# Kernel tuning notes

Measured on AMD Instinct MI355X. Metric: run time of the kernel, lower is better.

## Reference

```python
import jax, jax.numpy as jnp
import numpy as np

N_NODES = 100000
N_EDGES = 1000000
IN_FEATS = 64
HID = 128
NUM_CLASSES = 10


def setup_inputs() -> dict:
    key = jax.random.key(0)
    ks = jax.random.split(key, 8)
    x = jax.random.normal(ks[0], (N_NODES, IN_FEATS), dtype=jnp.float32)
    edge_index = jax.random.randint(ks[1], (2, N_EDGES), 0, N_NODES, dtype=jnp.int64)
    # Glorot-style init scale for weights
    def w(k, fan_in, fan_out):
        s = (2.0 / (fan_in + fan_out)) ** 0.5
        return jax.random.normal(k, (fan_in, fan_out), dtype=jnp.float32) * s
    return {
        "x": x,
        "edge_index": edge_index,
        "W1": w(ks[2], IN_FEATS, HID),
        "b1": jnp.zeros((HID,), dtype=jnp.float32),
        "W2": w(ks[3], HID, HID),
        "b2": jnp.zeros((HID,), dtype=jnp.float32),
        "Wl": w(ks[4], HID, NUM_CLASSES),
        "bl": jnp.zeros((NUM_CLASSES,), dtype=jnp.float32),
    }


def _gcn_conv(x, src, dst, norm, W, b, num_nodes):
    # PyG GCNConv: h = x W, then out_i = sum_{j->i} norm_ij * h_j + b
    h = x @ W  # [N, out]
    msgs = h[src] * norm[:, None]  # gather + scale  [E+N, out]
    out = jax.ops.segment_sum(msgs, dst, num_segments=num_nodes)
    return out + b


def reference(x, edge_index, W1, b1, W2, b2, Wl, bl):
    N = x.shape[0]
    loops = jnp.arange(N, dtype=edge_index.dtype)
    src = jnp.concatenate([edge_index[0], loops])  # source nodes (messages from)
    dst = jnp.concatenate([edge_index[1], loops])  # target nodes (aggregate at)
    # symmetric normalization: deg over targets (includes self-loops)
    deg = jax.ops.segment_sum(jnp.ones(dst.shape, dtype=x.dtype), dst, num_segments=N)
    dinv = jnp.where(deg > 0, jax.lax.rsqrt(deg), 0.0)
    norm = dinv[src] * dinv[dst]  # [E+N]

    h = jax.nn.relu(_gcn_conv(x, src, dst, norm, W1, b1, N))
    h = jax.nn.relu(_gcn_conv(h, src, dst, norm, W2, b2, N))
    return jax.nn.log_softmax(h @ Wl + bl, axis=1)
```

## Files before the change

kernel.cpp:

```cpp
#include <hip/hip_runtime.h>
#include <hip/hip_fp16.h>
#include <math.h>

#define NUM_CLASSES 10

#define BSH 7
#define BSZ 128
#define BCAP 1792
#define NBMAX 1024
#define P1BATCH 4096
#define PREPB 97

typedef _Float16 half8  __attribute__((ext_vector_type(8)));
typedef _Float16 half4t __attribute__((ext_vector_type(4)));
typedef float    floatx4 __attribute__((ext_vector_type(4)));

__global__ __launch_bounds__(256) void prep_p1_kernel(const float* __restrict__ W1,
                                                      const float* __restrict__ W2,
                                                      const float* __restrict__ Wlc,
                                                      _Float16* __restrict__ W1t,
                                                      _Float16* __restrict__ W2t,
                                                      _Float16* __restrict__ Wct,
                                                      const int* __restrict__ src,
                                                      const int* __restrict__ dst,
                                                      int* __restrict__ bucket_fill,
                                                      unsigned* __restrict__ pairs, int E) {
    __shared__ int hist[NBMAX], base[NBMAX], cur[NBMAX];
    const int tid = threadIdx.x;
    const int b = blockIdx.x;

    if (b < PREPB) {
        if (b < 32) {
            int i = b * 256 + tid;
            int k = i >> 7, c = i & 127;
            W1t[c * 72 + k] = (_Float16)W1[i];
        } else if (b < 96) {
            int i = (b - 32) * 256 + tid;
            int k = i >> 7, c = i & 127;
            W2t[c * 136 + k] = (_Float16)W2[i];
        } else {
            for (int i = tid; i < 16 * 136; i += 256) {
                int c = i / 136, k = i - c * 136;
                float v = (c < NUM_CLASSES && k < 128) ? Wlc[k * NUM_CLASSES + c] : 0.0f;
                Wct[i] = (_Float16)v;
            }
        }
        return;
    }

    for (int i = tid; i < NBMAX; i += 256) { hist[i] = 0; cur[i] = 0; }
    __syncthreads();
    const int bb = (b - PREPB) * P1BATCH;
    unsigned pk[16];
    int bk[16];
    int cnt = 0;
#pragma unroll
    for (int i = 0; i < 16; ++i) {
        int idx = bb + i * 256 + tid;
        if (idx < E) {
            int s = src[idx], d = dst[idx];
            bk[i] = d >> BSH;
            pk[i] = ((unsigned)s << BSH) | (unsigned)(d & (BSZ - 1));
            atomicAdd(&hist[bk[i]], 1);
            cnt = i + 1;
        }
    }
    __syncthreads();
    for (int i = tid; i < NBMAX; i += 256)
        if (hist[i] > 0) base[i] = atomicAdd(&bucket_fill[i], hist[i]);
    __syncthreads();
#pragma unroll
    for (int i = 0; i < 16; ++i) {
        if (i < cnt) {
            int bi = bk[i];
            int r = atomicAdd(&cur[bi], 1) + base[bi];
            if (r < BCAP) pairs[(size_t)bi * BCAP + r] = pk[i];
        }
    }
}

__global__ __launch_bounds__(256) void csr_p2_kernel(const int* __restrict__ bucket_fill,
                                                     const unsigned* __restrict__ pairs,
                                                     const float* __restrict__ x,
                                                     int* __restrict__ rowstart,
                                                     float* __restrict__ dinv,
                                                     int* __restrict__ csr_src,
                                                     __half2* __restrict__ xs_h,
                                                     int N, int nbuck) {
    __shared__ int cnt[BSZ], excl[BSZ], cur[BSZ];
    __shared__ int s1[256];
    const int tid = threadIdx.x;
    const int b = blockIdx.x;
    const int node0 = b << BSH;
    const int nodes_b = min(BSZ, N - node0);

    if (tid < BSZ) { cnt[tid] = 0; cur[tid] = 0; }
    int part = 0;
    for (int j = tid; j < b; j += 256) part += bucket_fill[j];
    s1[tid] = part;
    __syncthreads();
    for (int off = 128; off > 0; off >>= 1) {
        if (tid < off) s1[tid] += s1[tid + off];
        __syncthreads();
    }
    const int bbase = s1[0];
    const int ne = bucket_fill[b];
    __syncthreads();

    const unsigned* bp = pairs + (size_t)b * BCAP;
    for (int i = tid; i < ne; i += 256)
        atomicAdd(&cnt[bp[i] & (BSZ - 1)], 1);
    __syncthreads();
    int c = (tid < BSZ) ? cnt[tid] : 0;
    if (tid < BSZ) s1[tid] = c;
    __syncthreads();
    for (int off = 1; off < BSZ; off <<= 1) {
        int t = (tid < BSZ && tid >= off) ? s1[tid - off] : 0;
        __syncthreads();
        if (tid < BSZ) s1[tid] += t;
        __syncthreads();
    }
    if (tid < BSZ) excl[tid] = s1[tid] - c;
    __syncthreads();

    if (tid < nodes_b) {
        rowstart[node0 + tid] = bbase + excl[tid];
        dinv[node0 + tid] = rsqrtf((float)cnt[tid] + 1.0f);
    }
    if (b == nbuck - 1 && tid == 0) rowstart[N] = bbase + ne;

    for (int i = tid; i < nodes_b * 32; i += 256) {
        int ln = i >> 5;
        float d = rsqrtf((float)cnt[ln] + 1.0f);
        float2 v = ((const float2*)x)[(size_t)node0 * 32 + i];
        xs_h[(size_t)node0 * 32 + i] = __floats2half2_rn(v.x * d, v.y * d);
    }
    for (int i = tid; i < ne; i += 256) {
        unsigned p = bp[i];
        int d = (int)(p & (BSZ - 1));
        int r = atomicAdd(&cur[d], 1);
        csr_src[bbase + excl[d] + r] = (int)(p >> BSH);
    }
}

__global__ __launch_bounds__(256) void gather_gemm1_kernel(
        const __half2* __restrict__ xs,
        const float* __restrict__ dinv,
        const int* __restrict__ rowstart,
        const int* __restrict__ csr_src,
        const _Float16* __restrict__ Wt,
        const float* __restrict__ bias,
        _Float16* __restrict__ Out, int N) {
    constexpr int KP = 72;
    __shared__ _Float16 As[16 * KP];
    const int tid = threadIdx.x;
    const int lane = tid & 63;
    const int wave = tid >> 6;
    const int q = lane >> 4;
    const int l15 = lane & 15;

    half8 wfr[2][2];
    floatx4 bvr[2];
#pragma unroll
    for (int tt = 0; tt < 2; ++tt) {
        const int t = wave * 2 + tt;
#pragma unroll
        for (int c = 0; c < 2; ++c)
            wfr[tt][c] = *(const half8*)(Wt + (t * 16 + l15) * KP + c * 32 + q * 8);
        bvr[tt] = *(const floatx4*)(bias + t * 16 + q * 4);
    }

    const int f2 = lane & 31;
    for (int nn = 0; nn < 4; ++nn) {
        const int r = wave * 4 + nn;
        const int node = blockIdx.x * 16 + r;
        if (node < N) {
            int beg = rowstart[node];
            int end = rowstart[node + 1];
            int deg = end - beg;

            float2 self = __half22float2(xs[(size_t)node * 32 + f2]);
            float2 acc;

            if (deg <= 16) {
                int myidx = (lane < deg) ? csr_src[beg + lane] : node;
                float comp = (float)(deg - 15);
                acc.x = self.x * comp;
                acc.y = self.y * comp;
                float2 v[16];
#pragma unroll
                for (int u = 0; u < 16; ++u) {
                    int s = __shfl(myidx, u);
                    v[u] = __half22float2(xs[(size_t)s * 32 + f2]);
                }
#pragma unroll
                for (int u = 0; u < 16; ++u) { acc.x += v[u].x; acc.y += v[u].y; }
            } else {
                int lim = deg < 64 ? deg : 64;
                int myidx = (lane < lim) ? csr_src[beg + lane] : node;
                int itersUp = (lim + 7) & ~7;
                float comp = (float)(1 - (itersUp - lim));
                acc.x = self.x * comp;
                acc.y = self.y * comp;
                for (int j = 0; j < itersUp; j += 8) {
                    int s[8];
#pragma unroll
                    for (int u = 0; u < 8; ++u) s[u] = __shfl(myidx, j + u);
                    float2 v[8];
#pragma unroll
                    for (int u = 0; u < 8; ++u) v[u] = __half22float2(xs[(size_t)s[u] * 32 + f2]);
#pragma unroll
                    for (int u = 0; u < 8; ++u) { acc.x += v[u].x; acc.y += v[u].y; }
                }
                for (int j = beg + 64; j < end; ++j) {
                    float2 v = __half22float2(xs[(size_t)csr_src[j] * 32 + f2]);
                    acc.x += v.x;
                    acc.y += v.y;
                }
            }
            if (lane < 32) {
                float d = dinv[node];
                ((__half2*)As)[r * 36 + f2] = __floats2half2_rn(d * acc.x, d * acc.y);
            }
        }
    }
    __syncthreads();

    half8 xf[2];
#pragma unroll
    for (int c = 0; c < 2; ++c)
        xf[c] = *(const half8*)(As + l15 * KP + c * 32 + q * 8);
    const int myrow = blockIdx.x * 16 + l15;
    float sc = (myrow < N) ? dinv[myrow] : 0.0f;
#pragma unroll
    for (int tt = 0; tt < 2; ++tt) {
        floatx4 acc = (floatx4){0.f, 0.f, 0.f, 0.f};
#pragma unroll
        for (int c = 0; c < 2; ++c)
            acc = __builtin_amdgcn_mfma_f32_16x16x32_f16(wfr[tt][c], xf[c], acc, 0, 0, 0);
        if (myrow < N) {
            const int c0 = (wave * 2 + tt) * 16 + q * 4;
            half4t hh;
#pragma unroll
            for (int j = 0; j < 4; ++j)
                hh[j] = (_Float16)(sc * fmaxf(acc[j] + bvr[tt][j], 0.0f));
            *(half4t*)(Out + (size_t)myrow * 128 + c0) = hh;
        }
    }
}

__global__ __launch_bounds__(256) void gather_gemm_final_kernel(
        const __half2* __restrict__ hs,
        const float* __restrict__ dinv,
        const int* __restrict__ rowstart,
        const int* __restrict__ csr_src,
        const _Float16* __restrict__ Wt,
        const float* __restrict__ bias,
        const _Float16* __restrict__ Wct,
        const float* __restrict__ bl,
        float* __restrict__ out, int N) {
    constexpr int KP = 136;
    __shared__ _Float16 As[16 * KP];
    __shared__ _Float16 H2[16 * KP];
    const int tid = threadIdx.x;
    const int lane = tid & 63;
    const int wave = tid >> 6;
    const int q = lane >> 4;
    const int l15 = lane & 15;

    half8 wfr[2][4];
    floatx4 bvr[2];
#pragma unroll
    for (int tt = 0; tt < 2; ++tt) {
        const int t = wave * 2 + tt;
#pragma unroll
        for (int c = 0; c < 4; ++c)
            wfr[tt][c] = *(const half8*)(Wt + (t * 16 + l15) * KP + c * 32 + q * 8);
        bvr[tt] = *(const floatx4*)(bias + t * 16 + q * 4);
    }

    for (int nn = 0; nn < 4; ++nn) {
        const int r = wave * 4 + nn;
        const int node = blockIdx.x * 16 + r;
        if (node < N) {
            int beg = rowstart[node];
            int end = rowstart[node + 1];
            int deg = end - beg;

            float2 self = __half22float2(hs[(size_t)node * 64 + lane]);
            int lim = deg < 64 ? deg : 64;
            int myidx = (lane < lim) ? csr_src[beg + lane] : node;
            int itersUp = (lim + 7) & ~7;
            float comp = (float)(1 - (itersUp - lim));
            float2 acc;
            acc.x = self.x * comp;
            acc.y = self.y * comp;

            for (int j = 0; j < itersUp; j += 8) {
                int s[8];
#pragma unroll
                for (int u = 0; u < 8; ++u) s[u] = __shfl(myidx, j + u);
                float2 v[8];
#pragma unroll
                for (int u = 0; u < 8; ++u) v[u] = __half22float2(hs[(size_t)s[u] * 64 + lane]);
#pragma unroll
                for (int u = 0; u < 8; ++u) { acc.x += v[u].x; acc.y += v[u].y; }
            }
            for (int j = beg + 64; j < end; ++j) {
                float2 v = __half22float2(hs[(size_t)csr_src[j] * 64 + lane]);
                acc.x += v.x;
                acc.y += v.y;
            }
            float d = dinv[node];
            ((__half2*)As)[r * 68 + lane] = __floats2half2_rn(d * acc.x, d * acc.y);
        }
    }
    __syncthreads();

    half8 xf[4];
#pragma unroll
    for (int c = 0; c < 4; ++c)
        xf[c] = *(const half8*)(As + l15 * KP + c * 32 + q * 8);

#pragma unroll
    for (int tt = 0; tt < 2; ++tt) {
        const int t = wave * 2 + tt;
        floatx4 acc = (floatx4){0.f, 0.f, 0.f, 0.f};
#pragma unroll
        for (int c = 0; c < 4; ++c)
            acc = __builtin_amdgcn_mfma_f32_16x16x32_f16(wfr[tt][c], xf[c], acc, 0, 0, 0);
        const int c0 = t * 16 + q * 4;
        half4t hh;
#pragma unroll
        for (int j = 0; j < 4; ++j)
            hh[j] = (_Float16)fmaxf(acc[j] + bvr[tt][j], 0.0f);
        *(half4t*)&H2[l15 * KP + c0] = hh;
    }
    __syncthreads();

    if (wave == 0) {
        floatx4 lg = (floatx4){0.f, 0.f, 0.f, 0.f};
#pragma unroll
        for (int c = 0; c < 4; ++c) {
            half8 wcf = *(const half8*)(Wct + l15 * KP + c * 32 + q * 8);
            half8 af = *(const half8*)(H2 + l15 * KP + c * 32 + q * 8);
            lg = __builtin_amdgcn_mfma_f32_16x16x32_f16(wcf, af, lg, 0, 0, 0);
        }
        const int myrow = blockIdx.x * 16 + l15;
        if (myrow < N) {
            float v[4];
#pragma unroll
            for (int reg = 0; reg < 4; ++reg) {
                int cls = q * 4 + reg;
                v[reg] = lg[reg] + ((cls < NUM_CLASSES) ? bl[cls] : -1e30f);
            }
            float mx = fmaxf(fmaxf(v[0], v[1]), fmaxf(v[2], v[3]));
            mx = fmaxf(mx, __shfl_xor(mx, 16));
            mx = fmaxf(mx, __shfl_xor(mx, 32));
            float sm = expf(v[0] - mx) + expf(v[1] - mx) + expf(v[2] - mx) + expf(v[3] - mx);
            sm += __shfl_xor(sm, 16);
            sm += __shfl_xor(sm, 32);
            float lse = mx + logf(sm);
#pragma unroll
            for (int reg = 0; reg < 4; ++reg) {
                int cls = q * 4 + reg;
                if (cls < NUM_CLASSES)
                    out[(size_t)myrow * NUM_CLASSES + cls] = v[reg] - lse;
            }
        }
    }
}

extern "C" void kernel_launch(void* const* d_in, const int* in_sizes, int n_in,
                              void* d_out, int out_size, void* d_ws, size_t ws_size,
                              hipStream_t stream) {
    const float* x  = (const float*)d_in[0];
    const int*   ei = (const int*)d_in[1];
    const float* W1 = (const float*)d_in[2];
    const float* b1 = (const float*)d_in[3];
    const float* W2 = (const float*)d_in[4];
    const float* b2 = (const float*)d_in[5];
    const float* Wlc = (const float*)d_in[6];
    const float* bl = (const float*)d_in[7];
    float* out = (float*)d_out;

    const int N = in_sizes[0] / 64;
    const int E = in_sizes[1] / 2;
    const int* src = ei;
    const int* dst = ei + E;
    const int nbuck = (N + BSZ - 1) >> BSH;

    char* ws = (char*)d_ws;
    int*      bucket_fill = (int*)(ws + 0);
    int*      rowstart    = (int*)(ws + 4096);
    float*    dinv        = (float*)(ws + 524288);
    _Float16* W1t         = (_Float16*)(ws + 1048576);
    _Float16* W2t         = (_Float16*)(ws + 1069056);
    _Float16* Wct         = (_Float16*)(ws + 1103872);
    unsigned* pairs       = (unsigned*)(ws + 2097152);
    int*      csr_src     = (int*)(ws + 12582912);
    __half2*  xs_h        = (__half2*)(ws + 16777216);
    __half2*  a1_h        = (__half2*)(ws + 73400320);

    const int P1B = (E + P1BATCH - 1) / P1BATCH;
    const int FGB = (N + 15) / 16;

    hipMemsetAsync(bucket_fill, 0, nbuck * sizeof(int), stream);
    prep_p1_kernel<<<PREPB + P1B, 256, 0, stream>>>(W1, W2, Wlc, W1t, W2t, Wct,
                                                    src, dst, bucket_fill, pairs, E);
    csr_p2_kernel<<<nbuck, 256, 0, stream>>>(bucket_fill, pairs, x, rowstart, dinv,
                                             csr_src, xs_h, N, nbuck);

    gather_gemm1_kernel<<<FGB, 256, 0, stream>>>(xs_h, dinv, rowstart, csr_src,
                                                 W1t, b1, (_Float16*)a1_h, N);

    gather_gemm_final_kernel<<<FGB, 256, 0, stream>>>(a1_h, dinv, rowstart, csr_src,
                                                      W2t, b2, Wct, bl, out, N);
}
```

Measured before the change: 225.1 us.

## Stage GEMM weights into LDS via async global_load_lds and widen final kernel to 512 threads

Both gather+GEMM kernels now copy the transposed weight matrix into shared memory with global_load_lds DMA instead of holding weight fragments in registers. Weight fragments and bias are read per MFMA step. This lowers VGPR pressure during the latency-bound gather phase and lets the weight copy overlap it. The final kernel also doubles to 512 threads and 32 nodes per block, sharing one LDS weight copy across more nodes, at the cost of much more LDS per block (about 52KB), which may limit resident blocks.

```diff
diff --git a/kernel.cpp b/kernel.cpp
--- a/kernel.cpp
+++ b/kernel.cpp
@@ -14,6 +14,12 @@
 typedef _Float16 half8  __attribute__((ext_vector_type(8)));
 typedef _Float16 half4t __attribute__((ext_vector_type(4)));
 typedef float    floatx4 __attribute__((ext_vector_type(4)));
+
+__device__ __forceinline__ void gload_lds16(const void* g, void* l) {
+    __builtin_amdgcn_global_load_lds(
+        (const __attribute__((address_space(1))) unsigned int*)g,
+        (__attribute__((address_space(3))) unsigned int*)l, 16, 0, 0);
+}
 
 __global__ __launch_bounds__(256) void prep_p1_kernel(const float* __restrict__ W1,
                                                       const float* __restrict__ W2,
@@ -152,6 +158,7 @@
         const float* __restrict__ bias,
         _Float16* __restrict__ Out, int N) {
     constexpr int KP = 72;
+    __shared__ _Float16 Wl[128 * KP];
     __shared__ _Float16 As[16 * KP];
     const int tid = threadIdx.x;
     const int lane = tid & 63;
@@ -159,16 +166,8 @@
     const int q = lane >> 4;
     const int l15 = lane & 15;
 
-    half8 wfr[2][2];
-    floatx4 bvr[2];
-#pragma unroll
-    for (int tt = 0; tt < 2; ++tt) {
-        const int t = wave * 2 + tt;
-#pragma unroll
-        for (int c = 0; c < 2; ++c)
-            wfr[tt][c] = *(const half8*)(Wt + (t * 16 + l15) * KP + c * 32 + q * 8);
-        bvr[tt] = *(const floatx4*)(bias + t * 16 + q * 4);
-    }
+    for (int i = wave; i < 18; i += 4)
+        gload_lds16((const char*)Wt + i * 1024 + lane * 16, (char*)Wl + i * 1024);
 
     const int f2 = lane & 31;
     for (int nn = 0; nn < 4; ++nn) {
@@ -234,22 +233,26 @@
     float sc = (myrow < N) ? dinv[myrow] : 0.0f;
 #pragma unroll
     for (int tt = 0; tt < 2; ++tt) {
+        const int t = wave * 2 + tt;
         floatx4 acc = (floatx4){0.f, 0.f, 0.f, 0.f};
 #pragma unroll
-        for (int c = 0; c < 2; ++c)
-            acc = __builtin_amdgcn_mfma_f32_16x16x32_f16(wfr[tt][c], xf[c], acc, 0, 0, 0);
+        for (int c = 0; c < 2; ++c) {
+            half8 wf = *(const half8*)(Wl + (t * 16 + l15) * KP + c * 32 + q * 8);
+            acc = __builtin_amdgcn_mfma_f32_16x16x32_f16(wf, xf[c], acc, 0, 0, 0);
+        }
         if (myrow < N) {
-            const int c0 = (wave * 2 + tt) * 16 + q * 4;
+            floatx4 bv = *(const floatx4*)(bias + t * 16 + q * 4);
+            const int c0 = t * 16 + q * 4;
             half4t hh;
 #pragma unroll
             for (int j = 0; j < 4; ++j)
-                hh[j] = (_Float16)(sc * fmaxf(acc[j] + bvr[tt][j], 0.0f));
+                hh[j] = (_Float16)(sc * fmaxf(acc[j] + bv[j], 0.0f));
             *(half4t*)(Out + (size_t)myrow * 128 + c0) = hh;
         }
     }
 }
 
-__global__ __launch_bounds__(256) void gather_gemm_final_kernel(
+__global__ __launch_bounds__(512) void gather_gemm_final_kernel(
         const __half2* __restrict__ hs,
         const float* __restrict__ dinv,
         const int* __restrict__ rowstart,
@@ -260,28 +263,21 @@
         const float* __restrict__ bl,
         float* __restrict__ out, int N) {
     constexpr int KP = 136;
-    __shared__ _Float16 As[16 * KP];
-    __shared__ _Float16 H2[16 * KP];
+    __shared__ _Float16 Wl[128 * KP];
+    __shared__ _Float16 As[32 * KP];
+    __shared__ _Float16 H2[32 * KP];
     const int tid = threadIdx.x;
     const int lane = tid & 63;
     const int wave = tid >> 6;
     const int q = lane >> 4;
     const int l15 = lane & 15;
 
-    half8 wfr[2][4];
-    floatx4 bvr[2];
-#pragma unroll
-    for (int tt = 0; tt < 2; ++tt) {
-        const int t = wave * 2 + tt;
-#pragma unroll
-        for (int c = 0; c < 4; ++c)
-            wfr[tt][c] = *(const half8*)(Wt + (t * 16 + l15) * KP + c * 32 + q * 8);
-        bvr[tt] = *(const floatx4*)(bias + t * 16 + q * 4);
-    }
+    for (int i = wave; i < 34; i += 8)
+        gload_lds16((const char*)Wt + i * 1024 + lane * 16, (char*)Wl + i * 1024);
 
     for (int nn = 0; nn < 4; ++nn) {
         const int r = wave * 4 + nn;
-        const int node = blockIdx.x * 16 + r;
+        const int node = blockIdx.x * 32 + r;
         if (node < N) {
             int beg = rowstart[node];
             int end = rowstart[node + 1];
@@ -317,36 +313,40 @@
     }
     __syncthreads();
 
+    const int h = wave & 1;
     half8 xf[4];
 #pragma unroll
     for (int c = 0; c < 4; ++c)
-        xf[c] = *(const half8*)(As + l15 * KP + c * 32 + q * 8);
+        xf[c] = *(const half8*)(As + (h * 16 + l15) * KP + c * 32 + q * 8);
 
 #pragma unroll
     for (int tt = 0; tt < 2; ++tt) {
-        const int t = wave * 2 + tt;
+        const int t = (wave >> 1) + tt * 4;
         floatx4 acc = (floatx4){0.f, 0.f, 0.f, 0.f};
 #pragma unroll
-        for (int c = 0; c < 4; ++c)
-            acc = __builtin_amdgcn_mfma_f32_16x16x32_f16(wfr[tt][c], xf[c], acc, 0, 0, 0);
+        for (int c = 0; c < 4; ++c) {
+            half8 wf = *(const half8*)(Wl + (t * 16 + l15) * KP + c * 32 + q * 8);
+            acc = __builtin_amdgcn_mfma_f32_16x16x32_f16(wf, xf[c], acc, 0, 0, 0);
+        }
+        floatx4 bv = *(const floatx4*)(bias + t * 16 + q * 4);
         const int c0 = t * 16 + q * 4;
         half4t hh;
 #pragma unroll
         for (int j = 0; j < 4; ++j)
-            hh[j] = (_Float16)fmaxf(acc[j] + bvr[tt][j], 0.0f);
-        *(half4t*)&H2[l15 * KP + c0] = hh;
-    }
-    __syncthreads();
-
-    if (wave == 0) {
+            hh[j] = (_Float16)fmaxf(acc[j] + bv[j], 0.0f);
+        *(half4t*)&H2[(h * 16 + l15) * KP + c0] = hh;
+    }
+    __syncthreads();
+
+    if (wave < 2) {
         floatx4 lg = (floatx4){0.f, 0.f, 0.f, 0.f};
 #pragma unroll
         for (int c = 0; c < 4; ++c) {
             half8 wcf = *(const half8*)(Wct + l15 * KP + c * 32 + q * 8);
-            half8 af = *(const half8*)(H2 + l15 * KP + c * 32 + q * 8);
+            half8 af = *(const half8*)(H2 + (wave * 16 + l15) * KP + c * 32 + q * 8);
             lg = __builtin_amdgcn_mfma_f32_16x16x32_f16(wcf, af, lg, 0, 0, 0);
         }
-        const int myrow = blockIdx.x * 16 + l15;
+        const int myrow = blockIdx.x * 32 + wave * 16 + l15;
         if (myrow < N) {
             float v[4];
 #pragma unroll
@@ -403,7 +403,8 @@
     __half2*  a1_h        = (__half2*)(ws + 73400320);
 
     const int P1B = (E + P1BATCH - 1) / P1BATCH;
-    const int FGB = (N + 15) / 16;
+    const int F1B = (N + 15) / 16;
+    const int F2B = (N + 31) / 32;
 
     hipMemsetAsync(bucket_fill, 0, nbuck * sizeof(int), stream);
     prep_p1_kernel<<<PREPB + P1B, 256, 0, stream>>>(W1, W2, Wlc, W1t, W2t, Wct,
@@ -411,9 +412,9 @@
     csr_p2_kernel<<<nbuck, 256, 0, stream>>>(bucket_fill, pairs, x, rowstart, dinv,
                                              csr_src, xs_h, N, nbuck);
 
-    gather_gemm1_kernel<<<FGB, 256, 0, stream>>>(xs_h, dinv, rowstart, csr_src,
+    gather_gemm1_kernel<<<F1B, 256, 0, stream>>>(xs_h, dinv, rowstart, csr_src,
                                                  W1t, b1, (_Float16*)a1_h, N);
 
-    gather_gemm_final_kernel<<<FGB, 256, 0, stream>>>(a1_h, dinv, rowstart, csr_src,
+    gather_gemm_final_kernel<<<F2B, 512, 0, stream>>>(a1_h, dinv, rowstart, csr_src,
                                                       W2t, b2, Wct, bl, out, N);
 }
```

Measured after the change: 213.4 us. 1.06x faster.
